# Kernel tuning notes

Hardware: AMD Instinct MI355X
Metric: run time of the kernel (lower is better)

Reference implementation:

```python
import jax, jax.numpy as jnp
import numpy as np

BZ, SRC_LEN, TGT_LEN, DIM = 32, 1024, 1024, 512


def setup_inputs() -> dict:
    key = jax.random.key(0)
    k1, k2, k3, k4 = jax.random.split(key, 4)
    src = jax.random.normal(k1, (BZ, SRC_LEN, DIM), dtype=jnp.float32)
    tgt = jax.random.normal(k2, (BZ, TGT_LEN, DIM), dtype=jnp.float32)
    # lengths in [1, SRC_LEN] so every row has at least one valid position
    src_lengths = jax.random.randint(k3, (BZ,), 1, SRC_LEN + 1, dtype=jnp.int64)
    # nn.Linear(2*dim, dim, bias=False): weight shape (dim, 2*dim)
    bound = 1.0 / np.sqrt(2 * DIM)
    w_out = jax.random.uniform(k4, (DIM, 2 * DIM), dtype=jnp.float32,
                               minval=-bound, maxval=bound)
    return {"src": src, "tgt": tgt, "src_lengths": src_lengths, "w_out": w_out}


def reference(src, tgt, src_lengths, w_out):
    # dot-product attention scores: (bz, tgt_len, src_len)
    score = jnp.einsum("btd,bsd->bts", tgt, src)
    # mask out padded source positions (position >= length)
    valid = jnp.arange(src.shape[1])[None, :] < src_lengths[:, None]  # (bz, src_len)
    score = jnp.where(valid[:, None, :], score, -jnp.inf)
    align = jax.nn.softmax(score, axis=-1)
    # context: (bz, tgt_len, dim)
    c = jnp.einsum("bts,bsd->btd", align, src)
    concat_c = jnp.concatenate([c, tgt], axis=-1)  # (bz, tgt_len, 2*dim)
    attn_h = jnp.einsum("bte,de->btd", concat_c, w_out)
    return attn_h, align
```

## Files before the change

### kernel.cpp

```cpp
#include <hip/hip_runtime.h>
#include <hip/hip_bf16.h>

typedef __attribute__((ext_vector_type(4))) float  f32x4;
typedef __attribute__((ext_vector_type(4))) float  float4v;
typedef __attribute__((ext_vector_type(8))) short  bf16x8;
typedef __attribute__((ext_vector_type(4))) short  bf16x4;
typedef __attribute__((ext_vector_type(2))) unsigned int u32x2;

#define BZ   32
#define SLEN 1024
#define TLEN 1024
#define DIM  512
#define TILE 128
#define LP   40

#define PSEL 0x07060302u

__device__ __forceinline__ unsigned int fbits(float x) { return __builtin_bit_cast(unsigned int, x); }
__device__ __forceinline__ float fval(unsigned int u) { return __builtin_bit_cast(float, u); }

__device__ __forceinline__ unsigned short f2bf(float x) {
  unsigned int u = fbits(x);
  unsigned int r = u + 0x7FFFu + ((u >> 16) & 1u);
  return (unsigned short)(r >> 16);
}
__device__ __forceinline__ float bf2f(unsigned short h) { return fval(((unsigned int)h) << 16); }

__device__ __forceinline__ unsigned int packhi(float x0, float x1) {
  return __builtin_amdgcn_perm(fbits(x1), fbits(x0), PSEL);
}

__device__ __forceinline__ int get_len(const int* __restrict__ p, int b) {
  bool is64 = (p[1] == 0) && (p[3] == 0) && (p[5] == 0);
  return is64 ? p[2 * b] : p[b];
}

#define TLP 68
__global__ __launch_bounds__(256) void k_transpose(
    const float* __restrict__ src, unsigned short* __restrict__ srcT) {
  const int b  = blockIdx.z;
  const int s0 = blockIdx.x * 64;
  const int d0 = blockIdx.y * 64;
  __shared__ unsigned short tl[64 * TLP];
  const int tid = threadIdx.x;
#pragma unroll
  for (int r = 0; r < 4; ++r) {
    const int idx = tid + 256 * r;
    const int row = idx >> 4, c4 = idx & 15;
    float4v x = *(const float4v*)(src + ((size_t)(b * SLEN + s0 + row)) * DIM + d0 + c4 * 4);
    unsigned short* pp = tl + row * TLP + c4 * 4;
    pp[0] = f2bf(x[0]); pp[1] = f2bf(x[1]); pp[2] = f2bf(x[2]); pp[3] = f2bf(x[3]);
  }
  __syncthreads();
#pragma unroll
  for (int r = 0; r < 2; ++r) {
    const int idx  = tid + 256 * r;
    const int drow = idx >> 3, c8 = idx & 7;
    union { unsigned short u[8]; bf16x8 v; } pk;
#pragma unroll
    for (int j = 0; j < 8; ++j) pk.u[j] = tl[(c8 * 8 + j) * TLP + drow];
    *(bf16x8*)(srcT + ((size_t)(b * DIM + d0 + drow)) * SLEN + s0 + c8 * 8) = pk.v;
  }
}

__global__ __launch_bounds__(256) void k_prep_w(
    const float* __restrict__ w, unsigned short* __restrict__ wbf) {
  const size_t i = ((size_t)blockIdx.x * 256 + threadIdx.x) * 8;
  float4v x0 = *(const float4v*)(w + i);
  float4v x1 = *(const float4v*)(w + i + 4);
  union { unsigned short u[8]; bf16x8 v; } hi;
#pragma unroll
  for (int j = 0; j < 4; ++j) { hi.u[j] = f2bf(x0[j]); hi.u[4 + j] = f2bf(x1[j]); }
  *(bf16x8*)(wbf + i) = hi.v;
}

__global__ __launch_bounds__(256) void k_score(
    const float* __restrict__ tgt, const float* __restrict__ src,
    const int* __restrict__ lens, float* __restrict__ align_out) {
  const int b  = blockIdx.z;
  const int t0 = blockIdx.x * TILE;
  const int s0 = blockIdx.y * TILE;
  const int len = get_len(lens, b);
  if (s0 >= len) return;

  __shared__ short aHi[TILE * LP], aLo[TILE * LP], bHi[TILE * LP], bLo[TILE * LP];

  const int tid  = threadIdx.x;
  const int lane = tid & 63;
  const int wid  = tid >> 6;
  const int wt   = wid >> 1, wsd = wid & 1;
  const int g    = lane >> 4, r16 = lane & 15;

  f32x4 acc[4][4];
#pragma unroll
  for (int m = 0; m < 4; ++m)
#pragma unroll
    for (int n = 0; n < 4; ++n) acc[m][n] = (f32x4){0.f, 0.f, 0.f, 0.f};

  const float* tgtB = tgt + ((size_t)(b * TLEN + t0)) * DIM;
  const float* srcB = src + ((size_t)(b * SLEN + s0)) * DIM;
  const int srow = tid >> 3, sc4 = tid & 7;

  for (int k0 = 0; k0 < DIM; k0 += 32) {
#pragma unroll
    for (int r = 0; r < 4; ++r) {
      const int row = srow + 32 * r;
      float4v va = *(const float4v*)(tgtB + (size_t)row * DIM + k0 + sc4 * 4);
      float4v vb = *(const float4v*)(srcB + (size_t)row * DIM + k0 + sc4 * 4);
      u32x2 ah, al, bh, bl;
      ah[0] = packhi(va[0], va[1]); ah[1] = packhi(va[2], va[3]);
      bh[0] = packhi(vb[0], vb[1]); bh[1] = packhi(vb[2], vb[3]);
      float ra0 = va[0] - fval(fbits(va[0]) & 0xFFFF0000u);
      float ra1 = va[1] - fval(fbits(va[1]) & 0xFFFF0000u);
      float ra2 = va[2] - fval(fbits(va[2]) & 0xFFFF0000u);
      float ra3 = va[3] - fval(fbits(va[3]) & 0xFFFF0000u);
      float rb0 = vb[0] - fval(fbits(vb[0]) & 0xFFFF0000u);
      float rb1 = vb[1] - fval(fbits(vb[1]) & 0xFFFF0000u);
      float rb2 = vb[2] - fval(fbits(vb[2]) & 0xFFFF0000u);
      float rb3 = vb[3] - fval(fbits(vb[3]) & 0xFFFF0000u);
      al[0] = packhi(ra0, ra1); al[1] = packhi(ra2, ra3);
      bl[0] = packhi(rb0, rb1); bl[1] = packhi(rb2, rb3);
      const int o = row * LP + sc4 * 4;
      *(u32x2*)(aHi + o) = ah; *(u32x2*)(aLo + o) = al;
      *(u32x2*)(bHi + o) = bh; *(u32x2*)(bLo + o) = bl;
    }
    __syncthreads();
    bf16x8 fah[4], fal[4], fbh[4], fbl[4];
#pragma unroll
    for (int m = 0; m < 4; ++m) {
      const int row = wt * 64 + m * 16 + r16;
      fah[m] = *(const bf16x8*)(aHi + row * LP + g * 8);
      fal[m] = *(const bf16x8*)(aLo + row * LP + g * 8);
    }
#pragma unroll
    for (int n = 0; n < 4; ++n) {
      const int row = wsd * 64 + n * 16 + r16;
      fbh[n] = *(const bf16x8*)(bHi + row * LP + g * 8);
      fbl[n] = *(const bf16x8*)(bLo + row * LP + g * 8);
    }
#pragma unroll
    for (int m = 0; m < 4; ++m)
#pragma unroll
      for (int n = 0; n < 4; ++n) {
        acc[m][n] = __builtin_amdgcn_mfma_f32_16x16x32_bf16(fah[m], fbh[n], acc[m][n], 0, 0, 0);
        acc[m][n] = __builtin_amdgcn_mfma_f32_16x16x32_bf16(fal[m], fbh[n], acc[m][n], 0, 0, 0);
        acc[m][n] = __builtin_amdgcn_mfma_f32_16x16x32_bf16(fah[m], fbl[n], acc[m][n], 0, 0, 0);
      }
    __syncthreads();
  }
  float* outB = align_out + ((size_t)(b * TLEN + t0)) * SLEN + s0;
#pragma unroll
  for (int m = 0; m < 4; ++m) {
    const int tr = wt * 64 + m * 16 + g * 4;
#pragma unroll
    for (int n = 0; n < 4; ++n) {
      const int sc = wsd * 64 + n * 16 + r16;
#pragma unroll
      for (int r = 0; r < 4; ++r)
        outB[(size_t)(tr + r) * SLEN + sc] = acc[m][n][r];
    }
  }
}

__global__ __launch_bounds__(256) void k_softmax(
    const int* __restrict__ lens, float* __restrict__ align_io) {
  const int row  = blockIdx.x * 4 + (threadIdx.x >> 6);
  const int lane = threadIdx.x & 63;
  const int b    = row >> 10;
  const int len  = get_len(lens, b);
  float* p = align_io + (size_t)row * SLEN;
  float v[4][4];
  float mx = -3.0e38f;
#pragma unroll
  for (int q = 0; q < 4; ++q) {
    const int sb = (lane + 64 * q) * 4;
    float4v x = *(const float4v*)(p + sb);
#pragma unroll
    for (int j = 0; j < 4; ++j) {
      v[q][j] = x[j];
      if (sb + j < len) mx = fmaxf(mx, x[j]);
    }
  }
#pragma unroll
  for (int off = 1; off < 64; off <<= 1) mx = fmaxf(mx, __shfl_xor(mx, off));
  float sum = 0.f;
#pragma unroll
  for (int q = 0; q < 4; ++q) {
    const int sb = (lane + 64 * q) * 4;
#pragma unroll
    for (int j = 0; j < 4; ++j) {
      float e = (sb + j < len) ? __expf(v[q][j] - mx) : 0.f;
      v[q][j] = e; sum += e;
    }
  }
#pragma unroll
  for (int off = 1; off < 64; off <<= 1) sum += __shfl_xor(sum, off);
  const float inv = 1.f / sum;
#pragma unroll
  for (int q = 0; q < 4; ++q) {
    float4v x;
#pragma unroll
    for (int j = 0; j < 4; ++j) x[j] = v[q][j] * inv;
    *(float4v*)(p + (lane + 64 * q) * 4) = x;
  }
}

__global__ __launch_bounds__(256) void k_pv(
    const float* __restrict__ align_in, const unsigned short* __restrict__ srcT,
    const int* __restrict__ lens, unsigned short* __restrict__ cws) {
  const int b  = blockIdx.z;
  const int t0 = blockIdx.x * TILE;
  const int d0 = blockIdx.y * TILE;
  const int len = get_len(lens, b);
  const int ksteps = (len + 31) >> 5;

  __shared__ short A[TILE * LP], B[TILE * LP];
  const int tid  = threadIdx.x;
  const int lane = tid & 63;
  const int wid  = tid >> 6;
  const int wt   = wid >> 1, wsd = wid & 1;
  const int g    = lane >> 4, r16 = lane & 15;

  f32x4 acc[4][4];
#pragma unroll
  for (int m = 0; m < 4; ++m)
#pragma unroll
    for (int n = 0; n < 4; ++n) acc[m][n] = (f32x4){0.f, 0.f, 0.f, 0.f};

  for (int ks = 0; ks < ksteps; ++ks) {
    const int k0 = ks * 32;
#pragma unroll
    for (int r = 0; r < 4; ++r) {
      const int row = (tid >> 3) + 32 * r, c4 = tid & 7;
      float4v x = *(const float4v*)(align_in + ((size_t)(b * TLEN + t0 + row)) * SLEN + k0 + c4 * 4);
      u32x2 h;
      h[0] = packhi(x[0], x[1]); h[1] = packhi(x[2], x[3]);
      *(u32x2*)(A + row * LP + c4 * 4) = h;
    }
#pragma unroll
    for (int r = 0; r < 2; ++r) {
      const int row = (tid >> 2) + 64 * r, c8 = tid & 3;
      bf16x8 x = *(const bf16x8*)(srcT + ((size_t)(b * DIM + d0 + row)) * SLEN + k0 + c8 * 8);
      *(bf16x8*)(B + row * LP + c8 * 8) = x;
    }
    __syncthreads();
    bf16x8 fa[4], fb[4];
#pragma unroll
    for (int m = 0; m < 4; ++m) fa[m] = *(const bf16x8*)(A + (wt * 64 + m * 16 + r16) * LP + g * 8);
#pragma unroll
    for (int n = 0; n < 4; ++n) fb[n] = *(const bf16x8*)(B + (wsd * 64 + n * 16 + r16) * LP + g * 8);
#pragma unroll
    for (int m = 0; m < 4; ++m)
#pragma unroll
      for (int n = 0; n < 4; ++n)
        acc[m][n] = __builtin_amdgcn_mfma_f32_16x16x32_bf16(fa[m], fb[n], acc[m][n], 0, 0, 0);
    __syncthreads();
  }
#pragma unroll
  for (int m = 0; m < 4; ++m) {
    const int tr = wt * 64 + m * 16 + g * 4;
#pragma unroll
    for (int n = 0; n < 4; ++n) {
      const int dc = wsd * 64 + n * 16 + r16;
#pragma unroll
      for (int r = 0; r < 4; ++r)
        cws[((size_t)(b * TLEN + t0 + tr + r)) * DIM + d0 + dc] = f2bf(acc[m][n][r]);
    }
  }
}

__global__ __launch_bounds__(256) void k_proj(
    const unsigned short* __restrict__ cws, const float* __restrict__ tgt,
    const unsigned short* __restrict__ wbf, float* __restrict__ attn_out) {
  const int b  = blockIdx.z;
  const int t0 = blockIdx.x * TILE;
  const int d0 = blockIdx.y * TILE;

  __shared__ short A[TILE * LP], B[TILE * LP];
  const int tid  = threadIdx.x;
  const int lane = tid & 63;
  const int wid  = tid >> 6;
  const int wt   = wid >> 1, wsd = wid & 1;
  const int g    = lane >> 4, r16 = lane & 15;

  f32x4 acc[4][4];
#pragma unroll
  for (int m = 0; m < 4; ++m)
#pragma unroll
    for (int n = 0; n < 4; ++n) acc[m][n] = (f32x4){0.f, 0.f, 0.f, 0.f};

  for (int k0 = 0; k0 < 2 * DIM; k0 += 32) {
    if (k0 < DIM) {
#pragma unroll
      for (int r = 0; r < 2; ++r) {
        const int row = (tid >> 2) + 64 * r, c8 = tid & 3;
        bf16x8 x = *(const bf16x8*)(cws + ((size_t)(b * TLEN + t0 + row)) * DIM + k0 + c8 * 8);
        *(bf16x8*)(A + row * LP + c8 * 8) = x;
      }
    } else {
#pragma unroll
      for (int r = 0; r < 4; ++r) {
        const int row = (tid >> 3) + 32 * r, c4 = tid & 7;
        float4v x = *(const float4v*)(tgt + ((size_t)(b * TLEN + t0 + row)) * DIM + (k0 - DIM) + c4 * 4);
        bf16x4 h;
#pragma unroll
        for (int j = 0; j < 4; ++j) h[j] = (short)f2bf(x[j]);
        *(bf16x4*)(A + row * LP + c4 * 4) = h;
      }
    }
#pragma unroll
    for (int r = 0; r < 2; ++r) {
      const int row = (tid >> 2) + 64 * r, c8 = tid & 3;
      bf16x8 x = *(const bf16x8*)(wbf + ((size_t)(d0 + row)) * (2 * DIM) + k0 + c8 * 8);
      *(bf16x8*)(B + row * LP + c8 * 8) = x;
    }
    __syncthreads();
    bf16x8 fa[4], fb[4];
#pragma unroll
    for (int m = 0; m < 4; ++m) fa[m] = *(const bf16x8*)(A + (wt * 64 + m * 16 + r16) * LP + g * 8);
#pragma unroll
    for (int n = 0; n < 4; ++n) fb[n] = *(const bf16x8*)(B + (wsd * 64 + n * 16 + r16) * LP + g * 8);
#pragma unroll
    for (int m = 0; m < 4; ++m)
#pragma unroll
      for (int n = 0; n < 4; ++n)
        acc[m][n] = __builtin_amdgcn_mfma_f32_16x16x32_bf16(fa[m], fb[n], acc[m][n], 0, 0, 0);
    __syncthreads();
  }
#pragma unroll
  for (int m = 0; m < 4; ++m) {
    const int tr = wt * 64 + m * 16 + g * 4;
#pragma unroll
    for (int n = 0; n < 4; ++n) {
      const int dc = wsd * 64 + n * 16 + r16;
#pragma unroll
      for (int r = 0; r < 4; ++r)
        attn_out[((size_t)(b * TLEN + t0 + tr + r)) * DIM + d0 + dc] = acc[m][n][r];
    }
  }
}

extern "C" void kernel_launch(void* const* d_in, const int* in_sizes, int n_in,
                              void* d_out, int out_size, void* d_ws, size_t ws_size,
                              hipStream_t stream) {
  const float* src   = (const float*)d_in[0];
  const float* tgt   = (const float*)d_in[1];
  const int*   lens  = (const int*)d_in[2];
  const float* w_out = (const float*)d_in[3];

  float* attn_out  = (float*)d_out;
  float* align_out = attn_out + (size_t)BZ * TLEN * DIM;

  const size_t NE = (size_t)BZ * SLEN * DIM;
  const size_t NW = (size_t)DIM * 2 * DIM;
  unsigned short* srcT = (unsigned short*)d_ws;
  unsigned short* cws  = srcT + NE;
  unsigned short* wbf  = cws + NE;

  k_transpose<<<dim3(16, 8, BZ), 256, 0, stream>>>(src, srcT);
  k_prep_w<<<dim3((unsigned)(NW / 8 / 256)), 256, 0, stream>>>(w_out, wbf);
  k_score<<<dim3(8, 8, BZ), 256, 0, stream>>>(tgt, src, lens, align_out);
  k_softmax<<<dim3(BZ * TLEN / 4), 256, 0, stream>>>(lens, align_out);
  k_pv<<<dim3(8, 4, BZ), 256, 0, stream>>>(align_out, srcT, lens, cws);
  k_proj<<<dim3(8, 4, BZ), 256, 0, stream>>>(cws, tgt, wbf, attn_out);
}
```

Before: 286.2 us.

## Use persistent atomic work queue over valid score tiles

Adds a tiny prefix-sum kernel that counts the valid source tiles per batch. The score kernel becomes persistent: 768 blocks pull tile indices from an atomic counter, so only valid tiles are scheduled, instead of a full 8x8x32 grid in which masked blocks exit early. This is meant to remove the launch and scheduling cost of empty blocks and to balance load across CUs. In exchange it adds one extra launch, atomic contention, and a linear search per item. The counter is zeroed by k_count on every call.

```diff
diff --git a/kernel.cpp b/kernel.cpp
--- a/kernel.cpp
+++ b/kernel.cpp
@@ -33,6 +33,24 @@
 __device__ __forceinline__ int get_len(const int* __restrict__ p, int b) {
   bool is64 = (p[1] == 0) && (p[3] == 0) && (p[5] == 0);
   return is64 ? p[2 * b] : p[b];
+}
+
+__global__ __launch_bounds__(64) void k_count(
+    const int* __restrict__ lens, int* __restrict__ meta) {
+  const int lane = threadIdx.x;
+  int nt = 0;
+  if (lane < 32) {
+    const int len = get_len(lens, lane);
+    nt = ((len + 127) >> 7) * 8;
+  }
+  int v = nt;
+#pragma unroll
+  for (int off = 1; off < 32; off <<= 1) {
+    int o = __shfl_up(v, off);
+    if (lane >= off) v += o;
+  }
+  if (lane < 32) meta[lane + 1] = v;
+  if (lane == 0) { meta[0] = 0; meta[33] = 0; }
 }
 
 #define TLP 68
@@ -76,88 +94,101 @@
 
 __global__ __launch_bounds__(256) void k_score(
     const float* __restrict__ tgt, const float* __restrict__ src,
-    const int* __restrict__ lens, float* __restrict__ align_out) {
-  const int b  = blockIdx.z;
-  const int t0 = blockIdx.x * TILE;
-  const int s0 = blockIdx.y * TILE;
-  const int len = get_len(lens, b);
-  if (s0 >= len) return;
-
+    int* __restrict__ meta, float* __restrict__ align_out) {
   __shared__ short aHi[TILE * LP], aLo[TILE * LP], bHi[TILE * LP], bLo[TILE * LP];
+  __shared__ int sOffs[33];
+  __shared__ int sItem;
 
   const int tid  = threadIdx.x;
+  if (tid < 33) sOffs[tid] = meta[tid];
   const int lane = tid & 63;
   const int wid  = tid >> 6;
   const int wt   = wid >> 1, wsd = wid & 1;
   const int g    = lane >> 4, r16 = lane & 15;
-
-  f32x4 acc[4][4];
-#pragma unroll
-  for (int m = 0; m < 4; ++m)
-#pragma unroll
-    for (int n = 0; n < 4; ++n) acc[m][n] = (f32x4){0.f, 0.f, 0.f, 0.f};
-
-  const float* tgtB = tgt + ((size_t)(b * TLEN + t0)) * DIM;
-  const float* srcB = src + ((size_t)(b * SLEN + s0)) * DIM;
   const int srow = tid >> 3, sc4 = tid & 7;
-
-  for (int k0 = 0; k0 < DIM; k0 += 32) {
-#pragma unroll
-    for (int r = 0; r < 4; ++r) {
-      const int row = srow + 32 * r;
-      float4v va = *(const float4v*)(tgtB + (size_t)row * DIM + k0 + sc4 * 4);
-      float4v vb = *(const float4v*)(srcB + (size_t)row * DIM + k0 + sc4 * 4);
-      u32x2 ah, al, bh, bl;
-      ah[0] = packhi(va[0], va[1]); ah[1] = packhi(va[2], va[3]);
-      bh[0] = packhi(vb[0], vb[1]); bh[1] = packhi(vb[2], vb[3]);
-      float ra0 = va[0] - fval(fbits(va[0]) & 0xFFFF0000u);
-      float ra1 = va[1] - fval(fbits(va[1]) & 0xFFFF0000u);
-      float ra2 = va[2] - fval(fbits(va[2]) & 0xFFFF0000u);
-      float ra3 = va[3] - fval(fbits(va[3]) & 0xFFFF0000u);
-      float rb0 = vb[0] - fval(fbits(vb[0]) & 0xFFFF0000u);
-      float rb1 = vb[1] - fval(fbits(vb[1]) & 0xFFFF0000u);
-      float rb2 = vb[2] - fval(fbits(vb[2]) & 0xFFFF0000u);
-      float rb3 = vb[3] - fval(fbits(vb[3]) & 0xFFFF0000u);
-      al[0] = packhi(ra0, ra1); al[1] = packhi(ra2, ra3);
-      bl[0] = packhi(rb0, rb1); bl[1] = packhi(rb2, rb3);
-      const int o = row * LP + sc4 * 4;
-      *(u32x2*)(aHi + o) = ah; *(u32x2*)(aLo + o) = al;
-      *(u32x2*)(bHi + o) = bh; *(u32x2*)(bLo + o) = bl;
-    }
-    __syncthreads();
-    bf16x8 fah[4], fal[4], fbh[4], fbl[4];
+  __syncthreads();
+  const int total = sOffs[32];
+
+  for (;;) {
+    if (tid == 0) sItem = atomicAdd(meta + 33, 1);
+    __syncthreads();
+    const int item = sItem;
+    if (item >= total) break;
+
+    int b = 0;
+    while (sOffs[b + 1] <= item) ++b;
+    const int ntiles = (sOffs[b + 1] - sOffs[b]) >> 3;
+    int s_idx = item - sOffs[b], t_idx = 0;
+    while (s_idx >= ntiles) { s_idx -= ntiles; ++t_idx; }
+    const int t0 = t_idx * TILE, s0 = s_idx * TILE;
+
+    f32x4 acc[4][4];
+#pragma unroll
+    for (int m = 0; m < 4; ++m)
+#pragma unroll
+      for (int n = 0; n < 4; ++n) acc[m][n] = (f32x4){0.f, 0.f, 0.f, 0.f};
+
+    const float* tgtB = tgt + ((size_t)(b * TLEN + t0)) * DIM;
+    const float* srcB = src + ((size_t)(b * SLEN + s0)) * DIM;
+
+    for (int k0 = 0; k0 < DIM; k0 += 32) {
+#pragma unroll
+      for (int r = 0; r < 4; ++r) {
+        const int row = srow + 32 * r;
+        float4v va = *(const float4v*)(tgtB + (size_t)row * DIM + k0 + sc4 * 4);
+        float4v vb = *(const float4v*)(srcB + (size_t)row * DIM + k0 + sc4 * 4);
+        u32x2 ah, al, bh, bl;
+        ah[0] = packhi(va[0], va[1]); ah[1] = packhi(va[2], va[3]);
+        bh[0] = packhi(vb[0], vb[1]); bh[1] = packhi(vb[2], vb[3]);
+        float ra0 = va[0] - fval(fbits(va[0]) & 0xFFFF0000u);
+        float ra1 = va[1] - fval(fbits(va[1]) & 0xFFFF0000u);
+        float ra2 = va[2] - fval(fbits(va[2]) & 0xFFFF0000u);
+        float ra3 = va[3] - fval(fbits(va[3]) & 0xFFFF0000u);
+        float rb0 = vb[0] - fval(fbits(vb[0]) & 0xFFFF0000u);
+        float rb1 = vb[1] - fval(fbits(vb[1]) & 0xFFFF0000u);
+        float rb2 = vb[2] - fval(fbits(vb[2]) & 0xFFFF0000u);
+        float rb3 = vb[3] - fval(fbits(vb[3]) & 0xFFFF0000u);
+        al[0] = packhi(ra0, ra1); al[1] = packhi(ra2, ra3);
+        bl[0] = packhi(rb0, rb1); bl[1] = packhi(rb2, rb3);
+        const int o = row * LP + sc4 * 4;
+        *(u32x2*)(aHi + o) = ah; *(u32x2*)(aLo + o) = al;
+        *(u32x2*)(bHi + o) = bh; *(u32x2*)(bLo + o) = bl;
+      }
+      __syncthreads();
+      bf16x8 fah[4], fal[4], fbh[4], fbl[4];
+#pragma unroll
+      for (int m = 0; m < 4; ++m) {
+        const int row = wt * 64 + m * 16 + r16;
+        fah[m] = *(const bf16x8*)(aHi + row * LP + g * 8);
+        fal[m] = *(const bf16x8*)(aLo + row * LP + g * 8);
+      }
+#pragma unroll
+      for (int n = 0; n < 4; ++n) {
+        const int row = wsd * 64 + n * 16 + r16;
+        fbh[n] = *(const bf16x8*)(bHi + row * LP + g * 8);
+        fbl[n] = *(const bf16x8*)(bLo + row * LP + g * 8);
+      }
+#pragma unroll
+      for (int m = 0; m < 4; ++m)
+#pragma unroll
+        for (int n = 0; n < 4; ++n) {
+          acc[m][n] = __builtin_amdgcn_mfma_f32_16x16x32_bf16(fah[m], fbh[n], acc[m][n], 0, 0, 0);
+          acc[m][n] = __builtin_amdgcn_mfma_f32_16x16x32_bf16(fal[m], fbh[n], acc[m][n], 0, 0, 0);
+          acc[m][n] = __builtin_amdgcn_mfma_f32_16x16x32_bf16(fah[m], fbl[n], acc[m][n], 0, 0, 0);
+        }
+      __syncthreads();
+    }
+    float* outB = align_out + ((size_t)(b * TLEN + t0)) * SLEN + s0;
 #pragma unroll
     for (int m = 0; m < 4; ++m) {
-      const int row = wt * 64 + m * 16 + r16;
-      fah[m] = *(const bf16x8*)(aHi + row * LP + g * 8);
-      fal[m] = *(const bf16x8*)(aLo + row * LP + g * 8);
-    }
-#pragma unroll
-    for (int n = 0; n < 4; ++n) {
-      const int row = wsd * 64 + n * 16 + r16;
-      fbh[n] = *(const bf16x8*)(bHi + row * LP + g * 8);
-      fbl[n] = *(const bf16x8*)(bLo + row * LP + g * 8);
-    }
-#pragma unroll
-    for (int m = 0; m < 4; ++m)
+      const int tr = wt * 64 + m * 16 + g * 4;
 #pragma unroll
       for (int n = 0; n < 4; ++n) {
-        acc[m][n] = __builtin_amdgcn_mfma_f32_16x16x32_bf16(fah[m], fbh[n], acc[m][n], 0, 0, 0);
-        acc[m][n] = __builtin_amdgcn_mfma_f32_16x16x32_bf16(fal[m], fbh[n], acc[m][n], 0, 0, 0);
-        acc[m][n] = __builtin_amdgcn_mfma_f32_16x16x32_bf16(fah[m], fbl[n], acc[m][n], 0, 0, 0);
-      }
-    __syncthreads();
-  }
-  float* outB = align_out + ((size_t)(b * TLEN + t0)) * SLEN + s0;
-#pragma unroll
-  for (int m = 0; m < 4; ++m) {
-    const int tr = wt * 64 + m * 16 + g * 4;
-#pragma unroll
-    for (int n = 0; n < 4; ++n) {
-      const int sc = wsd * 64 + n * 16 + r16;
-#pragma unroll
-      for (int r = 0; r < 4; ++r)
-        outB[(size_t)(tr + r) * SLEN + sc] = acc[m][n][r];
+        const int sc = wsd * 64 + n * 16 + r16;
+#pragma unroll
+        for (int r = 0; r < 4; ++r)
+          outB[(size_t)(tr + r) * SLEN + sc] = acc[m][n][r];
+      }
     }
   }
 }
@@ -356,10 +387,12 @@
   unsigned short* srcT = (unsigned short*)d_ws;
   unsigned short* cws  = srcT + NE;
   unsigned short* wbf  = cws + NE;
-
+  int*            meta = (int*)(wbf + NW);
+
+  k_count<<<dim3(1), 64, 0, stream>>>(lens, meta);
   k_transpose<<<dim3(16, 8, BZ), 256, 0, stream>>>(src, srcT);
   k_prep_w<<<dim3((unsigned)(NW / 8 / 256)), 256, 0, stream>>>(w_out, wbf);
-  k_score<<<dim3(8, 8, BZ), 256, 0, stream>>>(tgt, src, lens, align_out);
+  k_score<<<dim3(768), 256, 0, stream>>>(tgt, src, meta, align_out);
   k_softmax<<<dim3(BZ * TLEN / 4), 256, 0, stream>>>(lens, align_out);
   k_pv<<<dim3(8, 4, BZ), 256, 0, stream>>>(align_out, srcT, lens, cws);
   k_proj<<<dim3(8, 4, BZ), 256, 0, stream>>>(cws, tgt, wbf, attn_out);
```

New measurement: 331.8 us. +15.9%, slower.

## Load MFMA operands directly from global memory, dropping LDS staging in GEMM kernels

Applied to the files above, without the earlier changes.

The score, PV and projection kernels now have each wave load its MFMA fragments straight from global memory into registers, converting to bf16 in registers. This removes the shared-memory tiles and both __syncthreads per k-step. The cost is lost cross-wave data sharing: each wave re-reads the rows it needs, so global/L2 traffic roughly doubles, and each lane issues 32-byte strided loads. Softmax also skips loading fully masked quarters of a row and zeroes masked values.

```diff
diff --git a/kernel.cpp b/kernel.cpp
--- a/kernel.cpp
+++ b/kernel.cpp
@@ -12,7 +12,6 @@
 #define TLEN 1024
 #define DIM  512
 #define TILE 128
-#define LP   40
 
 #define PSEL 0x07060302u
 
@@ -28,6 +27,30 @@
 
 __device__ __forceinline__ unsigned int packhi(float x0, float x1) {
   return __builtin_amdgcn_perm(fbits(x1), fbits(x0), PSEL);
+}
+
+__device__ __forceinline__ void cvt8(const float4v& x0, const float4v& x1,
+                                     bf16x8& hi, bf16x8& lo) {
+  union { unsigned int u[4]; bf16x8 v; } H, L;
+  H.u[0] = packhi(x0[0], x0[1]); H.u[1] = packhi(x0[2], x0[3]);
+  H.u[2] = packhi(x1[0], x1[1]); H.u[3] = packhi(x1[2], x1[3]);
+  float r0 = x0[0] - fval(fbits(x0[0]) & 0xFFFF0000u);
+  float r1 = x0[1] - fval(fbits(x0[1]) & 0xFFFF0000u);
+  float r2 = x0[2] - fval(fbits(x0[2]) & 0xFFFF0000u);
+  float r3 = x0[3] - fval(fbits(x0[3]) & 0xFFFF0000u);
+  float r4 = x1[0] - fval(fbits(x1[0]) & 0xFFFF0000u);
+  float r5 = x1[1] - fval(fbits(x1[1]) & 0xFFFF0000u);
+  float r6 = x1[2] - fval(fbits(x1[2]) & 0xFFFF0000u);
+  float r7 = x1[3] - fval(fbits(x1[3]) & 0xFFFF0000u);
+  L.u[0] = packhi(r0, r1); L.u[1] = packhi(r2, r3);
+  L.u[2] = packhi(r4, r5); L.u[3] = packhi(r6, r7);
+  hi = H.v; lo = L.v;
+}
+__device__ __forceinline__ bf16x8 cvt8hi(const float4v& x0, const float4v& x1) {
+  union { unsigned int u[4]; bf16x8 v; } H;
+  H.u[0] = packhi(x0[0], x0[1]); H.u[1] = packhi(x0[2], x0[3]);
+  H.u[2] = packhi(x1[0], x1[1]); H.u[3] = packhi(x1[2], x1[3]);
+  return H.v;
 }
 
 __device__ __forceinline__ int get_len(const int* __restrict__ p, int b) {
@@ -83,8 +106,6 @@
   const int len = get_len(lens, b);
   if (s0 >= len) return;
 
-  __shared__ short aHi[TILE * LP], aLo[TILE * LP], bHi[TILE * LP], bLo[TILE * LP];
-
   const int tid  = threadIdx.x;
   const int lane = tid & 63;
   const int wid  = tid >> 6;
@@ -97,47 +118,28 @@
 #pragma unroll
     for (int n = 0; n < 4; ++n) acc[m][n] = (f32x4){0.f, 0.f, 0.f, 0.f};
 
-  const float* tgtB = tgt + ((size_t)(b * TLEN + t0)) * DIM;
-  const float* srcB = src + ((size_t)(b * SLEN + s0)) * DIM;
-  const int srow = tid >> 3, sc4 = tid & 7;
+  const float* aB = tgt + ((size_t)(b * TLEN + t0 + wt * 64 + r16)) * DIM + g * 8;
+  const float* bB = src + ((size_t)(b * SLEN + s0 + wsd * 64 + r16)) * DIM + g * 8;
 
   for (int k0 = 0; k0 < DIM; k0 += 32) {
-#pragma unroll
-    for (int r = 0; r < 4; ++r) {
-      const int row = srow + 32 * r;
-      float4v va = *(const float4v*)(tgtB + (size_t)row * DIM + k0 + sc4 * 4);
-      float4v vb = *(const float4v*)(srcB + (size_t)row * DIM + k0 + sc4 * 4);
-      u32x2 ah, al, bh, bl;
-      ah[0] = packhi(va[0], va[1]); ah[1] = packhi(va[2], va[3]);
-      bh[0] = packhi(vb[0], vb[1]); bh[1] = packhi(vb[2], vb[3]);
-      float ra0 = va[0] - fval(fbits(va[0]) & 0xFFFF0000u);
-      float ra1 = va[1] - fval(fbits(va[1]) & 0xFFFF0000u);
-      float ra2 = va[2] - fval(fbits(va[2]) & 0xFFFF0000u);
-      float ra3 = va[3] - fval(fbits(va[3]) & 0xFFFF0000u);
-      float rb0 = vb[0] - fval(fbits(vb[0]) & 0xFFFF0000u);
-      float rb1 = vb[1] - fval(fbits(vb[1]) & 0xFFFF0000u);
-      float rb2 = vb[2] - fval(fbits(vb[2]) & 0xFFFF0000u);
-      float rb3 = vb[3] - fval(fbits(vb[3]) & 0xFFFF0000u);
-      al[0] = packhi(ra0, ra1); al[1] = packhi(ra2, ra3);
-      bl[0] = packhi(rb0, rb1); bl[1] = packhi(rb2, rb3);
-      const int o = row * LP + sc4 * 4;
-      *(u32x2*)(aHi + o) = ah; *(u32x2*)(aLo + o) = al;
-      *(u32x2*)(bHi + o) = bh; *(u32x2*)(bLo + o) = bl;
-    }
-    __syncthreads();
+    float4v la[4][2], lb[4][2];
+#pragma unroll
+    for (int m = 0; m < 4; ++m) {
+      const float* p = aB + (size_t)(m * 16) * DIM + k0;
+      la[m][0] = *(const float4v*)(p);
+      la[m][1] = *(const float4v*)(p + 4);
+    }
+#pragma unroll
+    for (int n = 0; n < 4; ++n) {
+      const float* p = bB + (size_t)(n * 16) * DIM + k0;
+      lb[n][0] = *(const float4v*)(p);
+      lb[n][1] = *(const float4v*)(p + 4);
+    }
     bf16x8 fah[4], fal[4], fbh[4], fbl[4];
 #pragma unroll
-    for (int m = 0; m < 4; ++m) {
-      const int row = wt * 64 + m * 16 + r16;
-      fah[m] = *(const bf16x8*)(aHi + row * LP + g * 8);
-      fal[m] = *(const bf16x8*)(aLo + row * LP + g * 8);
-    }
-#pragma unroll
-    for (int n = 0; n < 4; ++n) {
-      const int row = wsd * 64 + n * 16 + r16;
-      fbh[n] = *(const bf16x8*)(bHi + row * LP + g * 8);
-      fbl[n] = *(const bf16x8*)(bLo + row * LP + g * 8);
-    }
+    for (int m = 0; m < 4; ++m) cvt8(la[m][0], la[m][1], fah[m], fal[m]);
+#pragma unroll
+    for (int n = 0; n < 4; ++n) cvt8(lb[n][0], lb[n][1], fbh[n], fbl[n]);
 #pragma unroll
     for (int m = 0; m < 4; ++m)
 #pragma unroll
@@ -146,7 +148,6 @@
         acc[m][n] = __builtin_amdgcn_mfma_f32_16x16x32_bf16(fal[m], fbh[n], acc[m][n], 0, 0, 0);
         acc[m][n] = __builtin_amdgcn_mfma_f32_16x16x32_bf16(fah[m], fbl[n], acc[m][n], 0, 0, 0);
       }
-    __syncthreads();
   }
   float* outB = align_out + ((size_t)(b * TLEN + t0)) * SLEN + s0;
 #pragma unroll
@@ -173,11 +174,16 @@
   float mx = -3.0e38f;
 #pragma unroll
   for (int q = 0; q < 4; ++q) {
+    if (256 * q >= len) {
+#pragma unroll
+      for (int j = 0; j < 4; ++j) v[q][j] = 0.f;
+      continue;
+    }
     const int sb = (lane + 64 * q) * 4;
     float4v x = *(const float4v*)(p + sb);
 #pragma unroll
     for (int j = 0; j < 4; ++j) {
-      v[q][j] = x[j];
+      v[q][j] = (sb + j < len) ? x[j] : 0.f;
       if (sb + j < len) mx = fmaxf(mx, x[j]);
     }
   }
@@ -214,7 +220,6 @@
   const int len = get_len(lens, b);
   const int ksteps = (len + 31) >> 5;
 
-  __shared__ short A[TILE * LP], B[TILE * LP];
   const int tid  = threadIdx.x;
   const int lane = tid & 63;
   const int wid  = tid >> 6;
@@ -227,34 +232,27 @@
 #pragma unroll
     for (int n = 0; n < 4; ++n) acc[m][n] = (f32x4){0.f, 0.f, 0.f, 0.f};
 
+  const float*          aB = align_in + ((size_t)(b * TLEN + t0 + wt * 64 + r16)) * SLEN + g * 8;
+  const unsigned short* bB = srcT     + ((size_t)(b * DIM  + d0 + wsd * 64 + r16)) * SLEN + g * 8;
+
   for (int ks = 0; ks < ksteps; ++ks) {
     const int k0 = ks * 32;
-#pragma unroll
-    for (int r = 0; r < 4; ++r) {
-      const int row = (tid >> 3) + 32 * r, c4 = tid & 7;
-      float4v x = *(const float4v*)(align_in + ((size_t)(b * TLEN + t0 + row)) * SLEN + k0 + c4 * 4);
-      u32x2 h;
-      h[0] = packhi(x[0], x[1]); h[1] = packhi(x[2], x[3]);
-      *(u32x2*)(A + row * LP + c4 * 4) = h;
-    }
-#pragma unroll
-    for (int r = 0; r < 2; ++r) {
-      const int row = (tid >> 2) + 64 * r, c8 = tid & 3;
-      bf16x8 x = *(const bf16x8*)(srcT + ((size_t)(b * DIM + d0 + row)) * SLEN + k0 + c8 * 8);
-      *(bf16x8*)(B + row * LP + c8 * 8) = x;
-    }
-    __syncthreads();
     bf16x8 fa[4], fb[4];
 #pragma unroll
-    for (int m = 0; m < 4; ++m) fa[m] = *(const bf16x8*)(A + (wt * 64 + m * 16 + r16) * LP + g * 8);
-#pragma unroll
-    for (int n = 0; n < 4; ++n) fb[n] = *(const bf16x8*)(B + (wsd * 64 + n * 16 + r16) * LP + g * 8);
+    for (int m = 0; m < 4; ++m) {
+      const float* p = aB + (size_t)(m * 16) * SLEN + k0;
+      float4v x0 = *(const float4v*)(p);
+      float4v x1 = *(const float4v*)(p + 4);
+      fa[m] = cvt8hi(x0, x1);
+    }
+#pragma unroll
+    for (int n = 0; n < 4; ++n)
+      fb[n] = *(const bf16x8*)(bB + (size_t)(n * 16) * SLEN + k0);
 #pragma unroll
     for (int m = 0; m < 4; ++m)
 #pragma unroll
       for (int n = 0; n < 4; ++n)
         acc[m][n] = __builtin_amdgcn_mfma_f32_16x16x32_bf16(fa[m], fb[n], acc[m][n], 0, 0, 0);
-    __syncthreads();
   }
 #pragma unroll
   for (int m = 0; m < 4; ++m) {
@@ -276,7 +274,6 @@
   const int t0 = blockIdx.x * TILE;
   const int d0 = blockIdx.y * TILE;
 
-  __shared__ short A[TILE * LP], B[TILE * LP];
   const int tid  = threadIdx.x;
   const int lane = tid & 63;
   const int wid  = tid >> 6;
@@ -289,43 +286,33 @@
 #pragma unroll
     for (int n = 0; n < 4; ++n) acc[m][n] = (f32x4){0.f, 0.f, 0.f, 0.f};
 
+  const unsigned short* cB = cws + ((size_t)(b * TLEN + t0 + wt * 64 + r16)) * DIM + g * 8;
+  const float*          tB = tgt + ((size_t)(b * TLEN + t0 + wt * 64 + r16)) * DIM + g * 8;
+  const unsigned short* wB = wbf + ((size_t)(d0 + wsd * 64 + r16)) * (2 * DIM) + g * 8;
+
   for (int k0 = 0; k0 < 2 * DIM; k0 += 32) {
+    bf16x8 fa[4], fb[4];
     if (k0 < DIM) {
 #pragma unroll
-      for (int r = 0; r < 2; ++r) {
-        const int row = (tid >> 2) + 64 * r, c8 = tid & 3;
-        bf16x8 x = *(const bf16x8*)(cws + ((size_t)(b * TLEN + t0 + row)) * DIM + k0 + c8 * 8);
-        *(bf16x8*)(A + row * LP + c8 * 8) = x;
+      for (int m = 0; m < 4; ++m)
+        fa[m] = *(const bf16x8*)(cB + (size_t)(m * 16) * DIM + k0);
+    } else {
+#pragma unroll
+      for (int m = 0; m < 4; ++m) {
+        const float* p = tB + (size_t)(m * 16) * DIM + (k0 - DIM);
+        float4v x0 = *(const float4v*)(p);
+        float4v x1 = *(const float4v*)(p + 4);
+        fa[m] = cvt8hi(x0, x1);
       }
-    } else {
-#pragma unroll
-      for (int r = 0; r < 4; ++r) {
-        const int row = (tid >> 3) + 32 * r, c4 = tid & 7;
-        float4v x = *(const float4v*)(tgt + ((size_t)(b * TLEN + t0 + row)) * DIM + (k0 - DIM) + c4 * 4);
-        bf16x4 h;
-#pragma unroll
-        for (int j = 0; j < 4; ++j) h[j] = (short)f2bf(x[j]);
-        *(bf16x4*)(A + row * LP + c4 * 4) = h;
-      }
-    }
-#pragma unroll
-    for (int r = 0; r < 2; ++r) {
-      const int row = (tid >> 2) + 64 * r, c8 = tid & 3;
-      bf16x8 x = *(const bf16x8*)(wbf + ((size_t)(d0 + row)) * (2 * DIM) + k0 + c8 * 8);
-      *(bf16x8*)(B + row * LP + c8 * 8) = x;
-    }
-    __syncthreads();
-    bf16x8 fa[4], fb[4];
-#pragma unroll
-    for (int m = 0; m < 4; ++m) fa[m] = *(const bf16x8*)(A + (wt * 64 + m * 16 + r16) * LP + g * 8);
-#pragma unroll
-    for (int n = 0; n < 4; ++n) fb[n] = *(const bf16x8*)(B + (wsd * 64 + n * 16 + r16) * LP + g * 8);
+    }
+#pragma unroll
+    for (int n = 0; n < 4; ++n)
+      fb[n] = *(const bf16x8*)(wB + (size_t)(n * 16) * (2 * DIM) + k0);
 #pragma unroll
     for (int m = 0; m < 4; ++m)
 #pragma unroll
       for (int n = 0; n < 4; ++n)
         acc[m][n] = __builtin_amdgcn_mfma_f32_16x16x32_bf16(fa[m], fb[n], acc[m][n], 0, 0, 0);
-    __syncthreads();
   }
 #pragma unroll
   for (int m = 0; m < 4; ++m) {
```

Result: slower. 508.1 us (+77.5%).
